# Optimization experiments

Hardware: AMD Instinct MI355X
Metric: run time of the kernel (lower is better)

The kernel has to match this reference:

```python
import jax, jax.numpy as jnp
import numpy as np

N = 200_000      # nodes
DEG = 10         # edges per node (RadiusGraph max_num_neighbors=10, loop=True)
E = N * DEG
F0, F1 = 3, 20   # in features (pos), hidden
EPS = 1e-5       # PyG StdAggregation epsilon


def _glorot(k, shape):
    return jax.random.normal(k, shape, jnp.float32) / jnp.sqrt(jnp.float32(shape[-1]))


def setup_inputs() -> dict:
    key = jax.random.key(0)
    ks = jax.random.split(key, 20)
    x = jax.random.normal(ks[0], (N, F0), jnp.float32)
    # each node gets DEG incoming edges: dst structured, src random; first edge per node is a self-loop
    src = jax.random.randint(ks[1], (E,), 0, N, jnp.int32)
    dst = jnp.repeat(jnp.arange(N, dtype=jnp.int32), DEG)
    src = src.at[::DEG].set(jnp.arange(N, dtype=jnp.int32))  # self-loops
    edge_index = jnp.stack([src, dst])
    return {
        "x": x,
        "edge_index": edge_index,
        # conv1: PNAConv(3, 20)
        "w_pre1": _glorot(ks[2], (F0, 2 * F0)), "b_pre1": jnp.zeros((F0,), jnp.float32),
        "w_post1": _glorot(ks[3], (F1, 17 * F0)), "b_post1": jnp.zeros((F1,), jnp.float32),
        "w_lin1": _glorot(ks[4], (F1, F1)), "b_lin1": jnp.zeros((F1,), jnp.float32),
        # conv2: PNAConv(20, 20)
        "w_pre2": _glorot(ks[5], (F1, 2 * F1)), "b_pre2": jnp.zeros((F1,), jnp.float32),
        "w_post2": _glorot(ks[6], (F1, 17 * F1)), "b_post2": jnp.zeros((F1,), jnp.float32),
        "w_lin2": _glorot(ks[7], (F1, F1)), "b_lin2": jnp.zeros((F1,), jnp.float32),
        # final Linear(20, 1)
        "w_out": _glorot(ks[8], (1, F1)), "b_out": jnp.zeros((1,), jnp.float32),
    }


def _pna(x, src, dst, avg_lin, avg_log, w_pre, b_pre, w_post, b_post, w_lin, b_lin):
    n = x.shape[0]
    # message: pre_nn(x_i || x_j)
    h = jnp.concatenate([x[dst], x[src]], axis=-1)          # [E, 2F]
    m = h @ w_pre.T + b_pre                                 # [E, F]
    cnt = jax.ops.segment_sum(jnp.ones(dst.shape[0], jnp.float32), dst, num_segments=n)
    deg = jnp.maximum(cnt, 1.0)                             # [N]
    s = jax.ops.segment_sum(m, dst, num_segments=n)
    s2 = jax.ops.segment_sum(m * m, dst, num_segments=n)
    mean = s / deg[:, None]
    var = jax.nn.relu(s2 / deg[:, None] - mean * mean)
    std = jnp.sqrt(var + EPS)
    has = (cnt > 0.0)[:, None]
    mn = jnp.where(has, jax.ops.segment_min(m, dst, num_segments=n), 0.0)
    mx = jnp.where(has, jax.ops.segment_max(m, dst, num_segments=n), 0.0)
    agg = jnp.concatenate([mean, mn, mx, std], axis=-1)     # [N, 4F]
    # degree scalers: identity, amplification, attenuation, linear
    logd = jnp.log(deg + 1.0)[:, None]
    out = jnp.concatenate([agg,
                           agg * (logd / avg_log),
                           agg * (avg_log / logd),
                           agg * (deg / avg_lin)[:, None]], axis=-1)  # [N, 16F]
    out = jnp.concatenate([x, out], axis=-1)                # [N, 17F]
    out = out @ w_post.T + b_post                           # post_nn
    return out @ w_lin.T + b_lin                            # final tower mixer


def reference(x, edge_index, w_pre1, b_pre1, w_post1, b_post1, w_lin1, b_lin1,
              w_pre2, b_pre2, w_post2, b_post2, w_lin2, b_lin2, w_out, b_out):
    src, dst = edge_index[0], edge_index[1]
    n = x.shape[0]
    cnt = jax.ops.segment_sum(jnp.ones(dst.shape[0], jnp.float32), dst, num_segments=n)
    avg_lin = cnt.mean()                    # avg_deg['lin'] over the degree histogram
    avg_log = jnp.log(cnt + 1.0).mean()     # avg_deg['log']
    h = jax.nn.relu(_pna(x, src, dst, avg_lin, avg_log, w_pre1, b_pre1, w_post1, b_post1, w_lin1, b_lin1))
    h = jax.nn.relu(_pna(h, src, dst, avg_lin, avg_log, w_pre2, b_pre2, w_post2, b_post2, w_lin2, b_lin2))
    return h @ w_out.T + b_out              # [N, 1]
```

## Files before the change

kernel.cpp:

```cpp
#include <hip/hip_runtime.h>
#include <hip/hip_fp16.h>


#define N_NODES 200000
#define NPB 64
#define NBLK (N_NODES / NPB)

#define O_WD1  0
#define O_WA1  64
#define O_B1C  304
#define O_WD2  336
#define O_WA2  736
#define O_B2C  2336
#define O_B2H  4096
#define O_D2   2004096

__global__ __launch_bounds__(128) void fold_kernel(
    const float* __restrict__ w_pre1, const float* __restrict__ b_pre1,
    const float* __restrict__ w_post1, const float* __restrict__ b_post1,
    const float* __restrict__ w_lin1,  const float* __restrict__ b_lin1,
    const float* __restrict__ w_pre2, const float* __restrict__ b_pre2,
    const float* __restrict__ w_post2, const float* __restrict__ b_post2,
    const float* __restrict__ w_lin2,  const float* __restrict__ b_lin2,
    float* __restrict__ ws)
{
    __shared__ float wl1[20], wl2[20], c1[51], c2s[340];
    __shared__ float swa1[12], swa2[80], s1[3], s2[20];
    const int j = blockIdx.x;
    const int t = threadIdx.x;
    if (t < 20) { wl1[t] = w_lin1[j*20 + t]; wl2[t] = w_lin2[j*20 + t]; }
    __syncthreads();
    for (int c = t; c < 51; c += 128) {
        float a = 0.f;
        #pragma unroll
        for (int k = 0; k < 20; ++k) a += wl1[k] * w_post1[k*51 + c];
        c1[c] = a;
    }
    for (int c = t; c < 340; c += 128) {
        float a = 0.f;
        #pragma unroll
        for (int k = 0; k < 20; ++k) a += wl2[k] * w_post2[k*340 + c];
        c2s[c] = a;
    }
    __syncthreads();
    if (t < 12) swa1[t] = c1[3+t]  + c1[15+t]  + c1[27+t]  + c1[39+t];
    if (t < 80) swa2[t] = c2s[20+t] + c2s[100+t] + c2s[180+t] + c2s[260+t];
    __syncthreads();
    if (t < 3)  s1[t] = swa1[t] + swa1[3+t]  + swa1[6+t];
    if (t < 20) s2[t] = swa2[t] + swa2[20+t] + swa2[40+t];
    if (t < 12) ws[O_WA1 + j*12 + t] = swa1[t];
    if (t < 80) ws[O_WA2 + j*80 + t] = swa2[t];
    __syncthreads();
    if (t < 3) {
        float a = c1[t];
        #pragma unroll
        for (int r = 0; r < 3; ++r) a += s1[r] * w_pre1[r*6 + t];
        ws[O_WD1 + j*3 + t] = a;
    }
    if (t < 20) {
        float a = c2s[t];
        #pragma unroll
        for (int r = 0; r < 20; ++r) a += s2[r] * w_pre2[r*40 + t];
        ws[O_WD2 + j*20 + t] = a;
    }
    if (t == 0) {
        float a = b_lin1[j];
        #pragma unroll
        for (int k = 0; k < 20; ++k) a += wl1[k] * b_post1[k];
        #pragma unroll
        for (int r = 0; r < 3;  ++r) a += s1[r] * b_pre1[r];
        ws[O_B1C + j] = a;
        float b = b_lin2[j];
        #pragma unroll
        for (int k = 0; k < 20; ++k) b += wl2[k] * b_post2[k];
        #pragma unroll
        for (int r = 0; r < 20; ++r) b += s2[r] * b_pre2[r];
        ws[O_B2C + j] = b;
    }
}

__global__ __launch_bounds__(320) void k1_kernel(
    const float* __restrict__ x, const int* __restrict__ src,
    const float* __restrict__ w_pre1, const float* __restrict__ w_pre2,
    const float* __restrict__ ws,
    __half* __restrict__ b2h, float* __restrict__ d2)
{
    __shared__ float sM[NPB * 33];
    __shared__ float sAgg[NPB * 13];
    __shared__ float sH1[NPB * 21];
    const int t = threadIdx.x;
    const int node0 = blockIdx.x * NPB;

    #pragma unroll
    for (int p = 0; p < 2; ++p) {
        const int slot = p*320 + t;
        const int il = slot / 10, e = slot - il*10;
        const int sj = src[node0*10 + slot];
        const float xs0 = x[sj*3+0], xs1 = x[sj*3+1], xs2 = x[sj*3+2];
        #pragma unroll
        for (int ff = 0; ff < 3; ++ff) {
            sM[il*33 + e*3 + ff] =
                w_pre1[ff*6+3]*xs0 + w_pre1[ff*6+4]*xs1 + w_pre1[ff*6+5]*xs2;
        }
    }
    __syncthreads();

    if (t < 192) {
        const int il = t / 3, f = t - il*3;
        float sum = 0.f, sq = 0.f, mn = 1e30f, mx = -1e30f;
        #pragma unroll
        for (int e = 0; e < 10; ++e) {
            const float m = sM[il*33 + e*3 + f];
            sum += m; sq += m*m; mn = fminf(mn, m); mx = fmaxf(mx, m);
        }
        const float mean = sum * 0.1f;
        const float var  = fmaxf(sq * 0.1f - mean*mean, 0.f);
        sAgg[il*13 + 0 + f] = mean;
        sAgg[il*13 + 3 + f] = mn;
        sAgg[il*13 + 6 + f] = mx;
        sAgg[il*13 + 9 + f] = sqrtf(var + 1e-5f);
    }
    __syncthreads();

    const int wv = __builtin_amdgcn_readfirstlane(t >> 6);
    const int il = t & 63;
    const int node = node0 + il;
    const int f0 = wv * 4;

    float ag[12];
    #pragma unroll
    for (int k = 0; k < 12; ++k) ag[k] = sAgg[il*13 + k];
    const float xi0 = x[node*3+0], xi1 = x[node*3+1], xi2 = x[node*3+2];
    #pragma unroll
    for (int ff = 0; ff < 4; ++ff) {
        const int f = f0 + ff;
        float acc = ws[O_B1C + f]
            + ws[O_WD1 + f*3+0]*xi0 + ws[O_WD1 + f*3+1]*xi1 + ws[O_WD1 + f*3+2]*xi2;
        #pragma unroll
        for (int k = 0; k < 12; ++k) acc += ws[O_WA1 + f*12 + k] * ag[k];
        sH1[il*21 + f] = fmaxf(acc, 0.f);
    }
    __syncthreads();

    float hk[20];
    #pragma unroll
    for (int k = 0; k < 20; ++k) hk[k] = sH1[il*21 + k];
    float vb[4], vd[4];
    #pragma unroll
    for (int ff = 0; ff < 4; ++ff) {
        const int f = f0 + ff;
        float B = 0.f, D = ws[O_B2C + f];
        #pragma unroll
        for (int k = 0; k < 20; ++k) {
            B += w_pre2[f*40 + 20 + k] * hk[k];
            D += ws[O_WD2 + f*20 + k]  * hk[k];
        }
        vb[ff] = B; vd[ff] = D;
    }
    __half2* bp = reinterpret_cast<__half2*>(&b2h[node*20 + f0]);
    bp[0] = __floats2half2_rn(vb[0], vb[1]);
    bp[1] = __floats2half2_rn(vb[2], vb[3]);
    *(float4*)&d2[node*20 + f0] = make_float4(vd[0], vd[1], vd[2], vd[3]);
}

__global__ __launch_bounds__(320) void k2_kernel(
    const int* __restrict__ src, const float* __restrict__ ws,
    const __half* __restrict__ b2h, const float* __restrict__ d2,
    const float* __restrict__ w_out, const float* __restrict__ b_out,
    float* __restrict__ out)
{
    __shared__ float sAgg[NPB * 81];
    __shared__ int   sSrc[NPB * 10];
    __shared__ float sPart[320];
    const int t = threadIdx.x;
    const int node0 = blockIdx.x * NPB;

    sSrc[t]       = src[node0*10 + t];
    sSrc[320 + t] = src[node0*10 + 320 + t];
    __syncthreads();

    #pragma unroll
    for (int p = 0; p < 2; ++p) {
        const int idx = p*320 + t;
        const int il = idx / 10, fp = idx - il*10;
        const int f = 2*fp;
        float s0=0.f, s1=0.f, q0=0.f, q1=0.f;
        float mn0=1e30f, mn1=1e30f, mx0=-1e30f, mx1=-1e30f;
        #pragma unroll
        for (int e = 0; e < 10; ++e) {
            const int sj = sSrc[il*10 + e];
            const float2 b = __half22float2(*(const __half2*)&b2h[sj*20 + f]);
            s0 += b.x; q0 += b.x*b.x; mn0 = fminf(mn0, b.x); mx0 = fmaxf(mx0, b.x);
            s1 += b.y; q1 += b.y*b.y; mn1 = fminf(mn1, b.y); mx1 = fmaxf(mx1, b.y);
        }
        const float me0 = s0*0.1f, me1 = s1*0.1f;
        const float sd0 = sqrtf(fmaxf(q0*0.1f - me0*me0, 0.f) + 1e-5f);
        const float sd1 = sqrtf(fmaxf(q1*0.1f - me1*me1, 0.f) + 1e-5f);
        sAgg[il*81 + f]      = me0;  sAgg[il*81 + f + 1]      = me1;
        sAgg[il*81 + 20 + f] = mn0;  sAgg[il*81 + 20 + f + 1] = mn1;
        sAgg[il*81 + 40 + f] = mx0;  sAgg[il*81 + 40 + f + 1] = mx1;
        sAgg[il*81 + 60 + f] = sd0;  sAgg[il*81 + 60 + f + 1] = sd1;
    }
    __syncthreads();

    const int wv = __builtin_amdgcn_readfirstlane(t >> 6);
    const int il = t & 63;
    const int node = node0 + il;
    const int f0 = wv * 4;

    const float4 dd = *(const float4*)&d2[node*20 + f0];
    float acc0 = dd.x, acc1 = dd.y, acc2 = dd.z, acc3 = dd.w;
    #pragma unroll
    for (int k = 0; k < 80; ++k) {
        const float ag = sAgg[il*81 + k];
        acc0 += ws[O_WA2 + (f0+0)*80 + k] * ag;
        acc1 += ws[O_WA2 + (f0+1)*80 + k] * ag;
        acc2 += ws[O_WA2 + (f0+2)*80 + k] * ag;
        acc3 += ws[O_WA2 + (f0+3)*80 + k] * ag;
    }
    const float py = w_out[f0+0]*fmaxf(acc0, 0.f) + w_out[f0+1]*fmaxf(acc1, 0.f)
                   + w_out[f0+2]*fmaxf(acc2, 0.f) + w_out[f0+3]*fmaxf(acc3, 0.f);
    sPart[wv*64 + il] = py;
    __syncthreads();

    if (t < 64) {
        float y = b_out[0];
        #pragma unroll
        for (int v = 0; v < 5; ++v) y += sPart[v*64 + t];
        out[node0 + t] = y;
    }
}

extern "C" void kernel_launch(void* const* d_in, const int* in_sizes, int n_in,
                              void* d_out, int out_size, void* d_ws, size_t ws_size,
                              hipStream_t stream)
{
    const float* x       = (const float*)d_in[0];
    const int*   eidx    = (const int*)  d_in[1];
    const float* w_pre1  = (const float*)d_in[2];
    const float* b_pre1  = (const float*)d_in[3];
    const float* w_post1 = (const float*)d_in[4];
    const float* b_post1 = (const float*)d_in[5];
    const float* w_lin1  = (const float*)d_in[6];
    const float* b_lin1  = (const float*)d_in[7];
    const float* w_pre2  = (const float*)d_in[8];
    const float* b_pre2  = (const float*)d_in[9];
    const float* w_post2 = (const float*)d_in[10];
    const float* b_post2 = (const float*)d_in[11];
    const float* w_lin2  = (const float*)d_in[12];
    const float* b_lin2  = (const float*)d_in[13];
    const float* w_out   = (const float*)d_in[14];
    const float* b_out   = (const float*)d_in[15];
    float* out = (float*)d_out;
    float* ws  = (float*)d_ws;
    __half* b2h = (__half*)(ws + O_B2H);

    fold_kernel<<<20, 128, 0, stream>>>(w_pre1, b_pre1, w_post1, b_post1,
                                        w_lin1, b_lin1, w_pre2, b_pre2,
                                        w_post2, b_post2, w_lin2, b_lin2, ws);
    k1_kernel<<<NBLK, 320, 0, stream>>>(x, eidx, w_pre1, w_pre2, ws,
                                        b2h, ws + O_D2);
    k2_kernel<<<NBLK, 320, 0, stream>>>(eidx, ws, b2h, ws + O_D2,
                                        w_out, b_out, out);
}
```

Measured before the change: 64.21 us.

## Store D2 intermediate in fp16, hoist loads, use nontemporal memory ops

The per-node D2 intermediate (the dense part of the second layer's post-mixer) is now written and read as fp16 instead of fp32, halving its traffic between the two kernels. The self-node x loads in k1 and the D2 loads in k2 are moved to the top of each kernel so their latency overlaps the gather phase. Nontemporal loads and stores are used for the edge indices, intermediates and output to avoid polluting the cache. Rounding D2 to fp16 adds precision loss on a value that feeds directly into the layer-2 output.

```diff
diff --git a/kernel.cpp b/kernel.cpp
--- a/kernel.cpp
+++ b/kernel.cpp
@@ -13,7 +13,7 @@
 #define O_WA2  736
 #define O_B2C  2336
 #define O_B2H  4096
-#define O_D2   2004096
+#define O_D2H  2004096
 
 __global__ __launch_bounds__(128) void fold_kernel(
     const float* __restrict__ w_pre1, const float* __restrict__ b_pre1,
@@ -83,7 +83,7 @@
     const float* __restrict__ x, const int* __restrict__ src,
     const float* __restrict__ w_pre1, const float* __restrict__ w_pre2,
     const float* __restrict__ ws,
-    __half* __restrict__ b2h, float* __restrict__ d2)
+    __half* __restrict__ b2h, __half* __restrict__ d2h)
 {
     __shared__ float sM[NPB * 33];
     __shared__ float sAgg[NPB * 13];
@@ -91,11 +91,16 @@
     const int t = threadIdx.x;
     const int node0 = blockIdx.x * NPB;
 
+    const int pil = t & 63;
+    const float xi0 = x[(node0+pil)*3+0];
+    const float xi1 = x[(node0+pil)*3+1];
+    const float xi2 = x[(node0+pil)*3+2];
+
     #pragma unroll
     for (int p = 0; p < 2; ++p) {
         const int slot = p*320 + t;
         const int il = slot / 10, e = slot - il*10;
-        const int sj = src[node0*10 + slot];
+        const int sj = __builtin_nontemporal_load(&src[node0*10 + slot]);
         const float xs0 = x[sj*3+0], xs1 = x[sj*3+1], xs2 = x[sj*3+2];
         #pragma unroll
         for (int ff = 0; ff < 3; ++ff) {
@@ -130,7 +135,6 @@
     float ag[12];
     #pragma unroll
     for (int k = 0; k < 12; ++k) ag[k] = sAgg[il*13 + k];
-    const float xi0 = x[node*3+0], xi1 = x[node*3+1], xi2 = x[node*3+2];
     #pragma unroll
     for (int ff = 0; ff < 4; ++ff) {
         const int f = f0 + ff;
@@ -157,15 +161,18 @@
         }
         vb[ff] = B; vd[ff] = D;
     }
-    __half2* bp = reinterpret_cast<__half2*>(&b2h[node*20 + f0]);
-    bp[0] = __floats2half2_rn(vb[0], vb[1]);
-    bp[1] = __floats2half2_rn(vb[2], vb[3]);
-    *(float4*)&d2[node*20 + f0] = make_float4(vd[0], vd[1], vd[2], vd[3]);
+    union { __half2 h[2]; unsigned long long u; } pb, pd;
+    pb.h[0] = __floats2half2_rn(vb[0], vb[1]);
+    pb.h[1] = __floats2half2_rn(vb[2], vb[3]);
+    pd.h[0] = __floats2half2_rn(vd[0], vd[1]);
+    pd.h[1] = __floats2half2_rn(vd[2], vd[3]);
+    __builtin_nontemporal_store(pb.u, (unsigned long long*)&b2h[node*20 + f0]);
+    __builtin_nontemporal_store(pd.u, (unsigned long long*)&d2h[node*20 + f0]);
 }
 
 __global__ __launch_bounds__(320) void k2_kernel(
     const int* __restrict__ src, const float* __restrict__ ws,
-    const __half* __restrict__ b2h, const float* __restrict__ d2,
+    const __half* __restrict__ b2h, const __half* __restrict__ d2h,
     const float* __restrict__ w_out, const float* __restrict__ b_out,
     float* __restrict__ out)
 {
@@ -175,8 +182,14 @@
     const int t = threadIdx.x;
     const int node0 = blockIdx.x * NPB;
 
-    sSrc[t]       = src[node0*10 + t];
-    sSrc[320 + t] = src[node0*10 + 320 + t];
+    const int pil = t & 63;
+    const int pf0 = (t >> 6) * 4;
+    union { unsigned long long u; __half2 h[2]; } pdd;
+    pdd.u = __builtin_nontemporal_load(
+        (const unsigned long long*)&d2h[(node0+pil)*20 + pf0]);
+
+    sSrc[t]       = __builtin_nontemporal_load(&src[node0*10 + t]);
+    sSrc[320 + t] = __builtin_nontemporal_load(&src[node0*10 + 320 + t]);
     __syncthreads();
 
     #pragma unroll
@@ -205,11 +218,11 @@
 
     const int wv = __builtin_amdgcn_readfirstlane(t >> 6);
     const int il = t & 63;
-    const int node = node0 + il;
     const int f0 = wv * 4;
 
-    const float4 dd = *(const float4*)&d2[node*20 + f0];
-    float acc0 = dd.x, acc1 = dd.y, acc2 = dd.z, acc3 = dd.w;
+    const float2 d01 = __half22float2(pdd.h[0]);
+    const float2 d23 = __half22float2(pdd.h[1]);
+    float acc0 = d01.x, acc1 = d01.y, acc2 = d23.x, acc3 = d23.y;
     #pragma unroll
     for (int k = 0; k < 80; ++k) {
         const float ag = sAgg[il*81 + k];
@@ -227,7 +240,7 @@
         float y = b_out[0];
         #pragma unroll
         for (int v = 0; v < 5; ++v) y += sPart[v*64 + t];
-        out[node0 + t] = y;
+        __builtin_nontemporal_store(y, &out[node0 + t]);
     }
 }
 
@@ -254,12 +267,11 @@
     float* out = (float*)d_out;
     float* ws  = (float*)d_ws;
     __half* b2h = (__half*)(ws + O_B2H);
+    __half* d2h = (__half*)(ws + O_D2H);
 
     fold_kernel<<<20, 128, 0, stream>>>(w_pre1, b_pre1, w_post1, b_post1,
                                         w_lin1, b_lin1, w_pre2, b_pre2,
                                         w_post2, b_post2, w_lin2, b_lin2, ws);
-    k1_kernel<<<NBLK, 320, 0, stream>>>(x, eidx, w_pre1, w_pre2, ws,
-                                        b2h, ws + O_D2);
-    k2_kernel<<<NBLK, 320, 0, stream>>>(eidx, ws, b2h, ws + O_D2,
-                                        w_out, b_out, out);
-}
+    k1_kernel<<<NBLK, 320, 0, stream>>>(x, eidx, w_pre1, w_pre2, ws, b2h, d2h);
+    k2_kernel<<<NBLK, 320, 0, stream>>>(eidx, ws, b2h, d2h, w_out, b_out, out);
+}
```

Measured after the change: 66.40 us. 3.4% more time.
